# Optimization experiments

Measured on AMD Instinct MI355X. Metric: run time of the kernel, lower is better.

## Reference

```python
import jax, jax.numpy as jnp
import numpy as np

G, N, D = 512, 400, 128   # graphs, nodes per graph, feature dim
K = 200                   # max_node_num (cluster slots per graph)
DOUT = 512
DMID = DOUT // 16         # 32


def setup_inputs() -> dict:
    key = jax.random.key(0)
    ks = jax.random.split(key, 10)
    x = jax.random.normal(ks[0], (G, N, D), dtype=jnp.float32)
    cluster = jax.random.randint(ks[1], (G, N), 0, K, dtype=jnp.int32)
    true_score = jax.random.uniform(ks[2], (G // 2, 1), dtype=jnp.float32)
    # learned parameters
    W1 = jax.random.normal(ks[3], (D, D), dtype=jnp.float32) / np.sqrt(D)
    b1 = jnp.zeros((D,), jnp.float32)
    W2 = jax.random.normal(ks[4], (DMID, K * D), dtype=jnp.float32) / np.sqrt(K * D)
    b2 = jax.random.normal(ks[5], (DMID,), dtype=jnp.float32) * 0.01
    W3 = jax.random.normal(ks[6], (DOUT, DMID), dtype=jnp.float32) / np.sqrt(DMID)
    b3 = jnp.zeros((DOUT,), jnp.float32)
    return {"x": x, "cluster": cluster, "true_score": true_score,
            "W1": W1, "b1": b1, "W2": W2, "b2": b2, "W3": W3, "b3": b3}


def reference(x, cluster, true_score, W1, b1, W2, b2, W3, b3):
    g, n, d = x.shape
    # avg_pool over clusters (scatter-mean), vectorized across all graphs
    ids = (cluster + jnp.arange(g, dtype=cluster.dtype)[:, None] * K).reshape(-1)
    flat = x.reshape(g * n, d)
    sums = jax.ops.segment_sum(flat, ids, num_segments=g * K)          # [g*K, d]
    cnt = jax.ops.segment_sum(jnp.ones((g * n,), x.dtype), ids, num_segments=g * K)
    pooled = sums / jnp.maximum(cnt, 1.0)[:, None]                     # empty clusters -> 0
    # MLP_1: Linear(D, D) + ReLU, applied per pooled node
    h = jax.nn.relu(pooled @ W1 + b1)                                  # [g*K, d]
    # flatten pooled node set; MLP_2 truncated linear == full weight on zero-padded vec
    h = h.reshape(g, K * d)
    h = jax.nn.relu(h @ W2.T + b2)                                     # [g, 32]
    # MLP_3: Linear(32, 512) + ReLU
    h = jax.nn.relu(h @ W3.T + b3)                                     # [g, 512]
    # cosine similarity between consecutive graph pairs (eps=1e-6 clamp as torch)
    g1, g2 = h[0::2], h[1::2]
    eps = 1e-6
    n1 = jnp.maximum(jnp.sqrt(jnp.sum(g1 * g1, -1)), eps)
    n2 = jnp.maximum(jnp.sqrt(jnp.sum(g2 * g2, -1)), eps)
    scores = (jnp.sum(g1 * g2, -1) / (n1 * n2))[:, None]               # [g//2, 1]
    loss = jnp.mean((scores - true_score) ** 2)                        # MSELoss
    return loss
```

## Files before the change

### kernel.cpp

```cpp
#include <hip/hip_runtime.h>
#include <math.h>

#define G 512
#define N 400
#define D 128
#define K 200
#define DOUT 512
#define DMID 32
#define GK (G*K)
#define KD (K*D)
#define NCHUNK 200

#define SH  129
#define SW2 36

#define KQ 25

__device__ __forceinline__ float relu(float v) { return fmaxf(v, 0.0f); }

typedef __attribute__((ext_vector_type(8))) short short8b;
typedef __attribute__((ext_vector_type(16))) float floatx16;

__device__ __forceinline__ ushort f2bf(float f) {
  unsigned u = __float_as_uint(f);
  unsigned r = (u + 0x7FFFu + ((u >> 16) & 1u)) >> 16;
  return (ushort)r;
}
__device__ __forceinline__ float bf2f(ushort h) {
  return __uint_as_float(((unsigned)h) << 16);
}

__global__ __launch_bounds__(256) void w1prep(
    const float* __restrict__ W1, ushort* __restrict__ wh, ushort* __restrict__ wl) {
  const int idx = blockIdx.x * 256 + threadIdx.x;
  const int i = idx & 7, l = (idx >> 3) & 63, ks = (idx >> 9) & 7, nt = idx >> 12;
  const int k = ks * 16 + (l >> 5) * 8 + i;
  const int n = nt * 32 + (l & 31);
  const float v = W1[k * D + n];
  const ushort h = f2bf(v);
  wh[idx] = h;
  wl[idx] = f2bf(v - bf2f(h));
}

__global__ __launch_bounds__(256) void pool_gemm1_fused(
    const float* __restrict__ x, const int* __restrict__ cluster,
    const ushort* __restrict__ wh, const ushort* __restrict__ wl,
    const float* __restrict__ b1, float* __restrict__ h1) {
  __shared__ int s_ids[N];
  __shared__ int s_cnt[KQ];
  __shared__ int s_off[KQ + 1];
  __shared__ int s_cur[KQ];
  __shared__ int s_sorted[N];
  __shared__ ushort sAhi[8 * 64 * 8];
  __shared__ ushort sAlo[8 * 64 * 8];
  const int g = blockIdx.y;
  const int kb = blockIdx.x * KQ;
  const int tid = threadIdx.x;
  const int* cg = cluster + g * N;

  for (int i = tid; i < N; i += 256) s_ids[i] = cg[i];
  if (tid < KQ) { s_cnt[tid] = 0; s_cur[tid] = 0; }
  {
    short8b z;
#pragma unroll
    for (int e = 0; e < 8; ++e) z[e] = 0;
    for (int i = tid; i < 512; i += 256) {
      *(short8b*)&sAhi[i * 8] = z;
      *(short8b*)&sAlo[i * 8] = z;
    }
  }
  __syncthreads();

  for (int i = tid; i < N; i += 256) {
    const int id = s_ids[i] - kb;
    if ((unsigned)id < (unsigned)KQ) atomicAdd(&s_cnt[id], 1);
  }
  __syncthreads();

  if (tid < 64) {
    const int cv = (tid < KQ) ? s_cnt[tid] : 0;
    int c = cv;
#pragma unroll
    for (int off = 1; off < 32; off <<= 1) {
      const int t = __shfl_up(c, off);
      if (tid >= off) c += t;
    }
    if (tid < KQ) s_off[tid] = c - cv;
    if (tid == KQ - 1) s_off[KQ] = c;
  }
  __syncthreads();

  for (int i = tid; i < N; i += 256) {
    const int id = s_ids[i] - kb;
    if ((unsigned)id < (unsigned)KQ) {
      const int pos = atomicAdd(&s_cur[id], 1);
      s_sorted[s_off[id] + pos] = (id << 9) | i;
    }
  }
  __syncthreads();

  const int wv = tid >> 6, l = tid & 63;
  {
    const int kl0 = (wv * KQ) >> 2;
    const int kl1 = ((wv + 1) * KQ) >> 2;
    const float* xg = x + (size_t)g * N * D + l * 2;
    const int k0 = 2 * l;
    const int ksL = k0 >> 4, kqL = (k0 >> 3) & 1, i0 = k0 & 7;

#define PL_FLUSH(KL, AX, AY, INV)                                          \
    {                                                                      \
      const int blk = ksL * 64 + ((kqL * 32 + (KL)) ^ ksL);                \
      const float fx = (AX) * (INV), fy = (AY) * (INV);                    \
      const ushort hx = f2bf(fx), hy = f2bf(fy);                           \
      ushort2 hv; hv.x = hx; hv.y = hy;                                    \
      ushort2 lv;                                                          \
      lv.x = f2bf(fx - bf2f(hx)); lv.y = f2bf(fy - bf2f(hy));              \
      *(ushort2*)&sAhi[blk * 8 + i0] = hv;                                 \
      *(ushort2*)&sAlo[blk * 8 + i0] = lv;                                 \
    }

    if (kl1 > kl0) {
      const int i0g = s_off[kl0], i1g = s_off[kl1];
      if (i1g > i0g) {
        int prev = -1;
        float ax = 0.0f, ay = 0.0f;
        int pkA[8], pkB[8];
        float2 vA[8], vB[8];

#define PL_LOAD(PK, VV, BASE)                                              \
        {                                                                  \
          _Pragma("unroll")                                                \
          for (int j = 0; j < 8; ++j) {                                    \
            const int mi = ((BASE) + j < i1g) ? (BASE) + j : i1g - 1;      \
            PK[j] = s_sorted[mi];                                          \
          }                                                                \
          _Pragma("unroll")                                                \
          for (int j = 0; j < 8; ++j)                                      \
            VV[j] = *(const float2*)&xg[(size_t)(PK[j] & 511) * D];        \
        }

#define PL_PROC(PK, VV, BASE)                                              \
        {                                                                  \
          _Pragma("unroll")                                                \
          for (int j = 0; j < 8; ++j) {                                    \
            if ((BASE) + j < i1g) {                                        \
              const int id = PK[j] >> 9;                                   \
              if (id != prev) {                                            \
                if (prev >= 0) {                                           \
                  const float inv = 1.0f / (float)s_cnt[prev];             \
                  PL_FLUSH(prev, ax, ay, inv);                             \
                }                                                          \
                ax = VV[j].x; ay = VV[j].y; prev = id;                     \
              } else { ax += VV[j].x; ay += VV[j].y; }                     \
            }                                                              \
          }                                                                \
        }

        int base = i0g;
        PL_LOAD(pkA, vA, base);
        while (base < i1g) {
          if (base + 8 < i1g) PL_LOAD(pkB, vB, base + 8);
          PL_PROC(pkA, vA, base);
          base += 8;
          if (base >= i1g) break;
          if (base + 8 < i1g) PL_LOAD(pkA, vA, base + 8);
          PL_PROC(pkB, vB, base);
          base += 8;
        }
        if (prev >= 0) {
          const float inv = 1.0f / (float)s_cnt[prev];
          PL_FLUSH(prev, ax, ay, inv);
        }
#undef PL_LOAD
#undef PL_PROC
      }
    }
#undef PL_FLUSH
  }
  __syncthreads();

  floatx16 acc0;
#pragma unroll
  for (int e = 0; e < 16; ++e) acc0[e] = 0.0f;

  const ushort* whw = wh + (size_t)(wv * 8) * 64 * 8;
  const ushort* wlw = wl + (size_t)(wv * 8) * 64 * 8;

#pragma unroll 2
  for (int ks = 0; ks < 8; ++ks) {
    const int lx = l ^ ks;
    const short8b bh = *(const short8b*)&whw[(ks * 64 + l) * 8];
    const short8b bl = *(const short8b*)&wlw[(ks * 64 + l) * 8];
    const short8b ah = *(const short8b*)&sAhi[(ks * 64 + lx) * 8];
    const short8b al = *(const short8b*)&sAlo[(ks * 64 + lx) * 8];
    acc0 = __builtin_amdgcn_mfma_f32_32x32x16_bf16(ah, bh, acc0, 0, 0, 0);
    acc0 = __builtin_amdgcn_mfma_f32_32x32x16_bf16(ah, bl, acc0, 0, 0, 0);
    acc0 = __builtin_amdgcn_mfma_f32_32x32x16_bf16(al, bh, acc0, 0, 0, 0);
  }

  const int col = l & 31;
  const int n = wv * 32 + col;
  const float bias = b1[n];
  const int rbase = 4 * (l >> 5);
  float* hrow = h1 + ((size_t)g * K + kb) * D + n;
#pragma unroll
  for (int e = 0; e < 16; ++e) {
    const int row = (e & 3) + 8 * (e >> 2) + rbase;
    if (row < KQ) hrow[(size_t)row * D] = relu(acc0[e] + bias);
  }
}

__global__ __launch_bounds__(256) void gemm2_partial(
    const float* __restrict__ h1, const float* __restrict__ W2,
    float* __restrict__ partials) {
  extern __shared__ float smem[];
  float* sHt = smem;
  float* sWT = smem + 32 * SH;
  const int kc = blockIdx.x;
  const int gb = blockIdx.y;
  const int k0 = kc * 128, g0 = gb * 32;
  const int tid = threadIdx.x;

  for (int i = tid; i < 32 * 128; i += 256) {
    const int r = i >> 7, k = i & 127;
    sHt[r * SH + k] = h1[(size_t)(g0 + r) * KD + k0 + k];
  }
  for (int i = tid; i < 32 * 128; i += 256) {
    const int j = i >> 7, k = i & 127;
    sWT[k * SW2 + j] = W2[(size_t)j * KD + k0 + k];
  }
  __syncthreads();

  const int jt = tid & 7;
  const int gt = tid >> 3;
  float acc[4];
#pragma unroll
  for (int j = 0; j < 4; j++) acc[j] = 0.0f;

  for (int k = 0; k < 128; ++k) {
    const float h = sHt[gt * SH + k];
    const float4 w0 = *(const float4*)&sWT[k * SW2 + jt * 4];
    acc[0] = fmaf(h, w0.x, acc[0]); acc[1] = fmaf(h, w0.y, acc[1]);
    acc[2] = fmaf(h, w0.z, acc[2]); acc[3] = fmaf(h, w0.w, acc[3]);
  }

  float* pp = partials + ((size_t)kc * G + g0 + gt) * DMID + jt * 4;
  *(float4*)&pp[0] = make_float4(acc[0], acc[1], acc[2], acc[3]);
}

__global__ __launch_bounds__(256) void gemm2_reduce1(
    const float* __restrict__ partials, float* __restrict__ partials2) {
  const int idx = blockIdx.x * 256 + threadIdx.x;
  const int cg = blockIdx.y;
  float s = 0.0f;
  for (int c = cg * 25; c < cg * 25 + 25; ++c)
    s += partials[(size_t)c * G * DMID + idx];
  partials2[(size_t)cg * G * DMID + idx] = s;
}

__global__ __launch_bounds__(256) void gemm2_reduce2(
    const float* __restrict__ partials2, const float* __restrict__ b2,
    float* __restrict__ h2) {
  const int idx = blockIdx.x * 256 + threadIdx.x;
  const int j = idx & 31;
  float s = 0.0f;
#pragma unroll
  for (int c = 0; c < 8; ++c) s += partials2[(size_t)c * G * DMID + idx];
  h2[idx] = relu(s + b2[j]);
}

__global__ __launch_bounds__(256) void head_kernel(
    const float* __restrict__ h2, const float* __restrict__ W3,
    const float* __restrict__ b3, const float* __restrict__ ts,
    float* __restrict__ pair_sq) {
  __shared__ float sA[DMID], sB[DMID];
  __shared__ float rdot[4], rna[4], rnb[4];
  const int p = blockIdx.x;
  const int tid = threadIdx.x;
  if (tid < DMID) sA[tid] = h2[(size_t)(2 * p) * DMID + tid];
  else if (tid < 2 * DMID) sB[tid - DMID] = h2[(size_t)(2 * p + 1) * DMID + (tid - DMID)];
  __syncthreads();

  float dot = 0.0f, na = 0.0f, nb = 0.0f;
#pragma unroll
  for (int rep = 0; rep < 2; ++rep) {
    const int o = rep * 256 + tid;
    const float* w = W3 + (size_t)o * DMID;
    float accA = b3[o], accB = accA;
#pragma unroll
    for (int m = 0; m < DMID; m += 4) {
      const float4 wv = *(const float4*)&w[m];
      accA = fmaf(sA[m], wv.x, accA); accB = fmaf(sB[m], wv.x, accB);
      accA = fmaf(sA[m + 1], wv.y, accA); accB = fmaf(sB[m + 1], wv.y, accB);
      accA = fmaf(sA[m + 2], wv.z, accA); accB = fmaf(sB[m + 2], wv.z, accB);
      accA = fmaf(sA[m + 3], wv.w, accA); accB = fmaf(sB[m + 3], wv.w, accB);
    }
    const float a = relu(accA), b = relu(accB);
    dot = fmaf(a, b, dot); na = fmaf(a, a, na); nb = fmaf(b, b, nb);
  }
#pragma unroll
  for (int off = 32; off >= 1; off >>= 1) {
    dot += __shfl_down(dot, off);
    na  += __shfl_down(na, off);
    nb  += __shfl_down(nb, off);
  }
  const int wave = tid >> 6, lane = tid & 63;
  if (lane == 0) { rdot[wave] = dot; rna[wave] = na; rnb[wave] = nb; }
  __syncthreads();
  if (tid == 0) {
    const float dt = rdot[0] + rdot[1] + rdot[2] + rdot[3];
    const float nA = rna[0] + rna[1] + rna[2] + rna[3];
    const float nB = rnb[0] + rnb[1] + rnb[2] + rnb[3];
    const float n1 = fmaxf(sqrtf(nA), 1e-6f);
    const float n2 = fmaxf(sqrtf(nB), 1e-6f);
    const float sc = dt / (n1 * n2);
    const float e = sc - ts[p];
    pair_sq[p] = e * e;
  }
}

__global__ __launch_bounds__(256) void loss_kernel(
    const float* __restrict__ pair_sq, float* __restrict__ out) {
  __shared__ float red[4];
  const int tid = threadIdx.x;
  float v = pair_sq[tid];
#pragma unroll
  for (int off = 32; off >= 1; off >>= 1) v += __shfl_down(v, off);
  const int wave = tid >> 6, lane = tid & 63;
  if (lane == 0) red[wave] = v;
  __syncthreads();
  if (tid == 0) out[0] = (red[0] + red[1] + red[2] + red[3]) * (1.0f / 256.0f);
}

extern "C" void kernel_launch(void* const* d_in, const int* in_sizes, int n_in,
                              void* d_out, int out_size, void* d_ws, size_t ws_size,
                              hipStream_t stream) {
  const float* x       = (const float*)d_in[0];
  const int*   cluster = (const int*)d_in[1];
  const float* ts      = (const float*)d_in[2];
  const float* W1      = (const float*)d_in[3];
  const float* b1      = (const float*)d_in[4];
  const float* W2      = (const float*)d_in[5];
  const float* b2      = (const float*)d_in[6];
  const float* W3      = (const float*)d_in[7];
  const float* b3      = (const float*)d_in[8];

  float* ws = (float*)d_ws;
  float* h1        = ws;
  float* partials  = h1 + (size_t)GK * D;
  float* h2        = partials + (size_t)NCHUNK * G * DMID;
  float* pair_sq   = h2 + (size_t)G * DMID;
  float* partials2 = pair_sq + 256;
  ushort* wfrag_hi = (ushort*)(partials2 + 8 * G * DMID);
  ushort* wfrag_lo = wfrag_hi + 16384;

  w1prep<<<16384 / 256, 256, 0, stream>>>(W1, wfrag_hi, wfrag_lo);
  dim3 gridP(8, G);
  pool_gemm1_fused<<<gridP, 256, 0, stream>>>(x, cluster, wfrag_hi, wfrag_lo, b1, h1);
  dim3 gridC(NCHUNK, 16);
  gemm2_partial<<<gridC, 256, (32 * SH + 128 * SW2) * sizeof(float), stream>>>(h1, W2, partials);
  dim3 gridR1(G * DMID / 256, 8);
  gemm2_reduce1<<<gridR1, 256, 0, stream>>>(partials, partials2);
  gemm2_reduce2<<<G * DMID / 256, 256, 0, stream>>>(partials2, b2, h2);
  head_kernel<<<G / 2, 256, 0, stream>>>(h2, W3, b3, ts, pair_sq);
  loss_kernel<<<1, 256, 0, stream>>>(pair_sq, (float*)d_out);
}
```

Before: 89.58 us.

## Apply W1 before pooling and scatter-add GEMM outputs into LDS accumulators

The old kernel sorted nodes by cluster, averaged the gathered rows into pooled features, then ran the 128x128 GEMM on them. The new kernel uses linearity to multiply all 400 raw nodes per graph by W1 with MFMA. It stages row tiles with double-buffered register prefetch and atomically adds each output row into a per-cluster LDS accumulator. At the end it scales by 1/count, adds bias, and applies ReLU. This removes the sort and gather and gives coalesced x loads, but does 2x the GEMM FLOPs, adds many LDS atomics, and uses about 138KB of LDS per block with one block per graph.

```diff
diff --git a/kernel.cpp b/kernel.cpp
--- a/kernel.cpp
+++ b/kernel.cpp
@@ -14,7 +14,10 @@
 #define SH  129
 #define SW2 36
 
-#define KQ 25
+#define NT 13
+#define TPB 512
+
+#define G1_LDS (102400 + 16384 + 16384 + 1600 + 800 + 800)
 
 __device__ __forceinline__ float relu(float v) { return fmaxf(v, 0.0f); }
 
@@ -42,180 +45,137 @@
   wl[idx] = f2bf(v - bf2f(h));
 }
 
-__global__ __launch_bounds__(256) void pool_gemm1_fused(
+__global__ __launch_bounds__(TPB, 2) void gemm1_pool(
     const float* __restrict__ x, const int* __restrict__ cluster,
     const ushort* __restrict__ wh, const ushort* __restrict__ wl,
     const float* __restrict__ b1, float* __restrict__ h1) {
-  __shared__ int s_ids[N];
-  __shared__ int s_cnt[KQ];
-  __shared__ int s_off[KQ + 1];
-  __shared__ int s_cur[KQ];
-  __shared__ int s_sorted[N];
-  __shared__ ushort sAhi[8 * 64 * 8];
-  __shared__ ushort sAlo[8 * 64 * 8];
-  const int g = blockIdx.y;
-  const int kb = blockIdx.x * KQ;
+  extern __shared__ char smem[];
+  float*  s_acc = (float*)smem;
+  ushort* sAhi  = (ushort*)(smem + 102400);
+  ushort* sAlo  = sAhi + 2 * 8 * 64 * 8;
+  int*    s_ids = (int*)(smem + 102400 + 32768);
+  int*    s_cnt = s_ids + 400;
+  float*  s_inv = (float*)(s_cnt + 200);
+
+  const int g = blockIdx.x;
   const int tid = threadIdx.x;
-  const int* cg = cluster + g * N;
-
-  for (int i = tid; i < N; i += 256) s_ids[i] = cg[i];
-  if (tid < KQ) { s_cnt[tid] = 0; s_cur[tid] = 0; }
-  {
-    short8b z;
-#pragma unroll
-    for (int e = 0; e < 8; ++e) z[e] = 0;
-    for (int i = tid; i < 512; i += 256) {
-      *(short8b*)&sAhi[i * 8] = z;
-      *(short8b*)&sAlo[i * 8] = z;
-    }
-  }
-  __syncthreads();
-
-  for (int i = tid; i < N; i += 256) {
-    const int id = s_ids[i] - kb;
-    if ((unsigned)id < (unsigned)KQ) atomicAdd(&s_cnt[id], 1);
-  }
-  __syncthreads();
-
-  if (tid < 64) {
-    const int cv = (tid < KQ) ? s_cnt[tid] : 0;
-    int c = cv;
-#pragma unroll
-    for (int off = 1; off < 32; off <<= 1) {
-      const int t = __shfl_up(c, off);
-      if (tid >= off) c += t;
-    }
-    if (tid < KQ) s_off[tid] = c - cv;
-    if (tid == KQ - 1) s_off[KQ] = c;
-  }
-  __syncthreads();
-
-  for (int i = tid; i < N; i += 256) {
-    const int id = s_ids[i] - kb;
-    if ((unsigned)id < (unsigned)KQ) {
-      const int pos = atomicAdd(&s_cur[id], 1);
-      s_sorted[s_off[id] + pos] = (id << 9) | i;
-    }
-  }
-  __syncthreads();
-
-  const int wv = tid >> 6, l = tid & 63;
-  {
-    const int kl0 = (wv * KQ) >> 2;
-    const int kl1 = ((wv + 1) * KQ) >> 2;
-    const float* xg = x + (size_t)g * N * D + l * 2;
-    const int k0 = 2 * l;
-    const int ksL = k0 >> 4, kqL = (k0 >> 3) & 1, i0 = k0 & 7;
-
-#define PL_FLUSH(KL, AX, AY, INV)                                          \
-    {                                                                      \
-      const int blk = ksL * 64 + ((kqL * 32 + (KL)) ^ ksL);                \
-      const float fx = (AX) * (INV), fy = (AY) * (INV);                    \
-      const ushort hx = f2bf(fx), hy = f2bf(fy);                           \
-      ushort2 hv; hv.x = hx; hv.y = hy;                                    \
-      ushort2 lv;                                                          \
-      lv.x = f2bf(fx - bf2f(hx)); lv.y = f2bf(fy - bf2f(hy));              \
-      *(ushort2*)&sAhi[blk * 8 + i0] = hv;                                 \
-      *(ushort2*)&sAlo[blk * 8 + i0] = lv;                                 \
-    }
-
-    if (kl1 > kl0) {
-      const int i0g = s_off[kl0], i1g = s_off[kl1];
-      if (i1g > i0g) {
-        int prev = -1;
-        float ax = 0.0f, ay = 0.0f;
-        int pkA[8], pkB[8];
-        float2 vA[8], vB[8];
-
-#define PL_LOAD(PK, VV, BASE)                                              \
-        {                                                                  \
-          _Pragma("unroll")                                                \
-          for (int j = 0; j < 8; ++j) {                                    \
-            const int mi = ((BASE) + j < i1g) ? (BASE) + j : i1g - 1;      \
-            PK[j] = s_sorted[mi];                                          \
-          }                                                                \
-          _Pragma("unroll")                                                \
-          for (int j = 0; j < 8; ++j)                                      \
-            VV[j] = *(const float2*)&xg[(size_t)(PK[j] & 511) * D];        \
-        }
-
-#define PL_PROC(PK, VV, BASE)                                              \
-        {                                                                  \
-          _Pragma("unroll")                                                \
-          for (int j = 0; j < 8; ++j) {                                    \
-            if ((BASE) + j < i1g) {                                        \
-              const int id = PK[j] >> 9;                                   \
-              if (id != prev) {                                            \
-                if (prev >= 0) {                                           \
-                  const float inv = 1.0f / (float)s_cnt[prev];             \
-                  PL_FLUSH(prev, ax, ay, inv);                             \
-                }                                                          \
-                ax = VV[j].x; ay = VV[j].y; prev = id;                     \
-              } else { ax += VV[j].x; ay += VV[j].y; }                     \
-            }                                                              \
-          }                                                                \
-        }
-
-        int base = i0g;
-        PL_LOAD(pkA, vA, base);
-        while (base < i1g) {
-          if (base + 8 < i1g) PL_LOAD(pkB, vB, base + 8);
-          PL_PROC(pkA, vA, base);
-          base += 8;
-          if (base >= i1g) break;
-          if (base + 8 < i1g) PL_LOAD(pkA, vA, base + 8);
-          PL_PROC(pkB, vB, base);
-          base += 8;
-        }
-        if (prev >= 0) {
-          const float inv = 1.0f / (float)s_cnt[prev];
-          PL_FLUSH(prev, ax, ay, inv);
-        }
-#undef PL_LOAD
-#undef PL_PROC
+  const int lane = tid & 63;
+  const int w = tid >> 6;
+
+  const float* xg = x + (size_t)g * N * D;
+
+  const int urow = tid & 31, uc = tid >> 5;
+
+#define SLOAD(MT, R0, R1)                                                   \
+  {                                                                         \
+    int rr = (MT) * 32 + urow; rr = rr < N ? rr : N - 1;                    \
+    const float* p = xg + (size_t)rr * D + uc * 8;                          \
+    R0 = *(const float4*)p; R1 = *(const float4*)(p + 4);                   \
+  }
+
+#define SWRITE(BUF, R0, R1)                                                 \
+  {                                                                         \
+    float vv[8] = {R0.x, R0.y, R0.z, R0.w, R1.x, R1.y, R1.z, R1.w};         \
+    short8b hv, lv;                                                         \
+    _Pragma("unroll")                                                       \
+    for (int e = 0; e < 8; ++e) {                                           \
+      const ushort hh = f2bf(vv[e]);                                        \
+      hv[e] = (short)hh;                                                    \
+      lv[e] = (short)f2bf(vv[e] - bf2f(hh));                                \
+    }                                                                       \
+    const int di = (((BUF) * 8 + w) * 64 + lane) * 8;                       \
+    *(short8b*)&sAhi[di] = hv;                                              \
+    *(short8b*)&sAlo[di] = lv;                                              \
+  }
+
+  float4 Ra0, Ra1, Rb0, Rb1;
+  SLOAD(0, Ra0, Ra1);
+  SLOAD(1, Rb0, Rb1);
+  for (int i = tid; i < K * D / 4; i += TPB)
+    ((float4*)s_acc)[i] = make_float4(0.f, 0.f, 0.f, 0.f);
+  if (tid < K) s_cnt[tid] = 0;
+  __syncthreads();
+
+  if (tid < N) {
+    const int id = cluster[g * N + tid];
+    s_ids[tid] = id;
+    atomicAdd(&s_cnt[id], 1);
+  }
+  SWRITE(0, Ra0, Ra1);
+
+  const int nt = w & 3, ksbase = (w >> 2) * 4;
+  short8b Bh[4], Bl[4];
+#pragma unroll
+  for (int kk = 0; kk < 4; ++kk) {
+    const int ks = ksbase + kk;
+    Bh[kk] = *(const short8b*)&wh[((nt * 8 + ks) * 64 + lane) * 8];
+    Bl[kk] = *(const short8b*)&wl[((nt * 8 + ks) * 64 + lane) * 8];
+  }
+  __syncthreads();
+  if (tid < K) s_inv[tid] = 1.0f / (float)max(s_cnt[tid], 1);
+
+  const int col = lane & 31;
+  const int rbase4 = 4 * (lane >> 5);
+
+  for (int mt = 0; mt < NT; ++mt) {
+    const int buf = mt & 1;
+    if (mt + 1 < NT) {
+      if ((mt + 1) & 1) { SWRITE(1, Rb0, Rb1); } else { SWRITE(0, Ra0, Ra1); }
+    }
+    if (mt + 2 < NT) {
+      if (mt & 1) { SLOAD(mt + 2, Rb0, Rb1); } else { SLOAD(mt + 2, Ra0, Ra1); }
+    }
+
+    floatx16 acc;
+#pragma unroll
+    for (int e = 0; e < 16; ++e) acc[e] = 0.0f;
+
+    const ushort* ah0 = &sAhi[((buf * 8 + ksbase) * 64 + lane) * 8];
+    const ushort* al0 = &sAlo[((buf * 8 + ksbase) * 64 + lane) * 8];
+#pragma unroll
+    for (int kk = 0; kk < 4; ++kk) {
+      const short8b ah = *(const short8b*)&ah0[kk * 512];
+      const short8b al = *(const short8b*)&al0[kk * 512];
+      acc = __builtin_amdgcn_mfma_f32_32x32x16_bf16(ah, Bh[kk], acc, 0, 0, 0);
+      acc = __builtin_amdgcn_mfma_f32_32x32x16_bf16(ah, Bl[kk], acc, 0, 0, 0);
+      acc = __builtin_amdgcn_mfma_f32_32x32x16_bf16(al, Bh[kk], acc, 0, 0, 0);
+    }
+
+    const int rowbase = mt * 32 + rbase4;
+#pragma unroll
+    for (int e = 0; e < 16; ++e) {
+      const int r = rowbase + (e & 3) + 8 * (e >> 2);
+      if (r < N) {
+        const int id = s_ids[r];
+        atomicAdd(&s_acc[id * D + nt * 32 + col], acc[e]);
       }
     }
-#undef PL_FLUSH
-  }
-  __syncthreads();
-
-  floatx16 acc0;
-#pragma unroll
-  for (int e = 0; e < 16; ++e) acc0[e] = 0.0f;
-
-  const ushort* whw = wh + (size_t)(wv * 8) * 64 * 8;
-  const ushort* wlw = wl + (size_t)(wv * 8) * 64 * 8;
-
-#pragma unroll 2
-  for (int ks = 0; ks < 8; ++ks) {
-    const int lx = l ^ ks;
-    const short8b bh = *(const short8b*)&whw[(ks * 64 + l) * 8];
-    const short8b bl = *(const short8b*)&wlw[(ks * 64 + l) * 8];
-    const short8b ah = *(const short8b*)&sAhi[(ks * 64 + lx) * 8];
-    const short8b al = *(const short8b*)&sAlo[(ks * 64 + lx) * 8];
-    acc0 = __builtin_amdgcn_mfma_f32_32x32x16_bf16(ah, bh, acc0, 0, 0, 0);
-    acc0 = __builtin_amdgcn_mfma_f32_32x32x16_bf16(ah, bl, acc0, 0, 0, 0);
-    acc0 = __builtin_amdgcn_mfma_f32_32x32x16_bf16(al, bh, acc0, 0, 0, 0);
-  }
-
-  const int col = l & 31;
-  const int n = wv * 32 + col;
-  const float bias = b1[n];
-  const int rbase = 4 * (l >> 5);
-  float* hrow = h1 + ((size_t)g * K + kb) * D + n;
-#pragma unroll
-  for (int e = 0; e < 16; ++e) {
-    const int row = (e & 3) + 8 * (e >> 2) + rbase;
-    if (row < KQ) hrow[(size_t)row * D] = relu(acc0[e] + bias);
-  }
+    __syncthreads();
+  }
+
+  float* og = h1 + (size_t)g * KD;
+  for (int i = tid; i < K * D / 4; i += TPB) {
+    const int row = i >> 5;
+    const float iv = s_inv[row];
+    const float4 a = ((const float4*)s_acc)[i];
+    const float4 bb = *(const float4*)&b1[(i & 31) * 4];
+    float4 o;
+    o.x = relu(fmaf(a.x, iv, bb.x));
+    o.y = relu(fmaf(a.y, iv, bb.y));
+    o.z = relu(fmaf(a.z, iv, bb.z));
+    o.w = relu(fmaf(a.w, iv, bb.w));
+    ((float4*)og)[i] = o;
+  }
+#undef SLOAD
+#undef SWRITE
 }
 
 __global__ __launch_bounds__(256) void gemm2_partial(
     const float* __restrict__ h1, const float* __restrict__ W2,
     float* __restrict__ partials) {
-  extern __shared__ float smem[];
-  float* sHt = smem;
-  float* sWT = smem + 32 * SH;
+  extern __shared__ float smemf[];
+  float* sHt = smemf;
+  float* sWT = smemf + 32 * SH;
   const int kc = blockIdx.x;
   const int gb = blockIdx.y;
   const int k0 = kc * 128, g0 = gb * 32;
@@ -354,9 +314,16 @@
   ushort* wfrag_hi = (ushort*)(partials2 + 8 * G * DMID);
   ushort* wfrag_lo = wfrag_hi + 16384;
 
+  static bool attr_set = false;
+  if (!attr_set) {
+    (void)hipFuncSetAttribute((const void*)gemm1_pool,
+                              hipFuncAttributeMaxDynamicSharedMemorySize,
+                              160 * 1024);
+    attr_set = true;
+  }
+
   w1prep<<<16384 / 256, 256, 0, stream>>>(W1, wfrag_hi, wfrag_lo);
-  dim3 gridP(8, G);
-  pool_gemm1_fused<<<gridP, 256, 0, stream>>>(x, cluster, wfrag_hi, wfrag_lo, b1, h1);
+  gemm1_pool<<<G, TPB, G1_LDS, stream>>>(x, cluster, wfrag_hi, wfrag_lo, b1, h1);
   dim3 gridC(NCHUNK, 16);
   gemm2_partial<<<gridC, 256, (32 * SH + 128 * SW2) * sizeof(float), stream>>>(h1, W2, partials);
   dim3 gridR1(G * DMID / 256, 8);
```

After: 346.4 us. 287% more time.
